# Kernel tuning notes

Hardware: AMD Instinct MI355X
Metric: run time of the kernel (lower is better)

The kernel has to match this reference:

```python
import jax, jax.numpy as jnp
import numpy as np

NUM_Q = 1000
B, T = 64, 100
DK, DV, N = 128, 128, 128

def setup_inputs() -> dict:
    key = jax.random.key(0)
    ks = jax.random.split(key, 12)
    return {
        "q": jax.random.randint(ks[0], (B, T), 0, NUM_Q),
        "r": jax.random.randint(ks[1], (B, T), 0, 2),
        "k_emb": jax.random.normal(ks[2], (NUM_Q, DK), jnp.float32) * 0.1,
        "v_emb": jax.random.normal(ks[3], (2 * NUM_Q, DV), jnp.float32) * 0.1,
        "Mk": jax.random.normal(ks[4], (DK, N), jnp.float32) * 0.1,
        "Mv0": jax.random.normal(ks[5], (N, DV), jnp.float32) * 0.1,
        "f_W": jax.random.normal(ks[6], (2 * DK, DK), jnp.float32) * 0.05,
        "f_b": jnp.zeros((DK,), jnp.float32),
        "p_W": jax.random.normal(ks[7], (DK, 1), jnp.float32) * 0.05,
        "p_b": jnp.zeros((1,), jnp.float32),
        "e_W": jax.random.normal(ks[8], (DV, DV), jnp.float32) * 0.05,
        "e_b": jnp.zeros((DV,), jnp.float32),
        "a_W": jax.random.normal(ks[9], (DV, DV), jnp.float32) * 0.05,
        "a_b": jnp.zeros((DV,), jnp.float32),
    }

def reference(q, r, k_emb, v_emb, Mk, Mv0, f_W, f_b, p_W, p_b, e_W, e_b, a_W, a_b):
    num_q = k_emb.shape[0]
    qr = q + num_q * r                                    # [B,T]
    K = k_emb[q].transpose(1, 0, 2)                       # [T,B,DK]
    V = v_emb[qr].transpose(1, 0, 2)                      # [T,B,DV]
    Mvt0 = jnp.broadcast_to(Mv0, (q.shape[0],) + Mv0.shape)  # [B,N,DV]

    def step(Mvt, kv):
        kt, vt = kv                                       # [B,DK],[B,DV]
        wt = jax.nn.softmax(kt @ Mk, axis=-1)             # [B,N] attention weights
        rt = jnp.einsum('bn,bnd->bd', wt, Mvt)            # memory read
        ft = jnp.tanh(jnp.concatenate([rt, kt], axis=-1) @ f_W + f_b)
        pt = jax.nn.sigmoid(ft @ p_W + p_b)               # [B,1]
        et = jax.nn.sigmoid(vt @ e_W + e_b)               # erase gate [B,DV]
        at = jnp.tanh(vt @ a_W + a_b)                     # add vector [B,DV]
        w_ = wt[:, :, None]                               # [B,N,1]
        Mvt = Mvt * (1.0 - w_ * et[:, None, :]) + w_ * at[:, None, :]
        return Mvt, (pt, Mvt)

    _, (p, Mv) = jax.lax.scan(step, Mvt0, (K, V))         # p: [T,B,1], Mv: [T,B,N,DV]
    p = p.reshape(-1, 1)                                  # cat over time, dim=0 -> [T*B,1]
    Mv = Mv.reshape(-1, Mv.shape[-2], Mv.shape[-1])       # [T*B,N,DV]
    return p, Mv
```

## Files before the change

kernel.cpp:

```cpp
#include <hip/hip_runtime.h>
#include <stdint.h>
#include <stddef.h>


constexpr int B = 64;
constexpr int T = 100;
constexpr int D = 128;
constexpr int NUM_Q = 1000;
constexpr int G = 4;
constexpr int BT = B * T;
constexpr int WSTRIDE = BT * D;

__device__ __forceinline__ float sigmoidf_(float x) {
  return 1.0f / (1.0f + __expf(-x));
}

__global__ __launch_bounds__(128) void kernelA(
    const int* __restrict__ q, const int* __restrict__ r,
    const float* __restrict__ k_emb, const float* __restrict__ v_emb,
    const float* __restrict__ Mk,
    const float* __restrict__ f_W, const float* __restrict__ f_b,
    const float* __restrict__ e_W, const float* __restrict__ e_b,
    const float* __restrict__ a_W, const float* __restrict__ a_b,
    float* __restrict__ ws_w, float* __restrict__ ws_e,
    float* __restrict__ ws_a, float* __restrict__ ws_f)
{
  const int tid = threadIdx.x;
  const int b  = blockIdx.x / (T / G);
  const int tg = blockIdx.x % (T / G);
  const int tbase = tg * G;

  __shared__ float kt[G][D];
  __shared__ float vt[G][D];
  __shared__ float red[D];

  #pragma unroll
  for (int g = 0; g < G; ++g) {
    int idx = b * T + tbase + g;
    int qi  = q[idx];
    int qri = qi + NUM_Q * r[idx];
    kt[g][tid] = k_emb[qi * D + tid];
    vt[g][tid] = v_emb[qri * D + tid];
  }
  __syncthreads();

  float lg[G], se[G], sa[G], sf[G];
  #pragma unroll
  for (int g = 0; g < G; ++g) { lg[g] = 0.f; se[g] = 0.f; sa[g] = 0.f; sf[g] = 0.f; }

  #pragma unroll 4
  for (int k = 0; k < D; ++k) {
    float mk = Mk[k * D + tid];
    float ew = e_W[k * D + tid];
    float aw = a_W[k * D + tid];
    float fw = f_W[(D + k) * D + tid];
    #pragma unroll
    for (int g = 0; g < G; ++g) {
      float kk = kt[g][k];
      float vv = vt[g][k];
      lg[g] = fmaf(kk, mk, lg[g]);
      se[g] = fmaf(vv, ew, se[g]);
      sa[g] = fmaf(vv, aw, sa[g]);
      sf[g] = fmaf(kk, fw, sf[g]);
    }
  }

  const float eb = e_b[tid];
  const float ab = a_b[tid];
  const float fb = f_b[tid];

  for (int g = 0; g < G; ++g) {
    red[tid] = lg[g];
    __syncthreads();
    #pragma unroll
    for (int s = 64; s > 0; s >>= 1) {
      if (tid < s) red[tid] = fmaxf(red[tid], red[tid + s]);
      __syncthreads();
    }
    float mx = red[0];
    __syncthreads();
    float ex = __expf(lg[g] - mx);
    red[tid] = ex;
    __syncthreads();
    #pragma unroll
    for (int s = 64; s > 0; s >>= 1) {
      if (tid < s) red[tid] += red[tid + s];
      __syncthreads();
    }
    float sm = red[0];
    __syncthreads();

    int idx = (b * T + tbase + g) * D + tid;
    ws_w[idx] = ex / sm;
    ws_e[idx] = sigmoidf_(se[g] + eb);
    ws_a[idx] = tanhf(sa[g] + ab);
    ws_f[idx] = sf[g] + fb;
  }
}

__global__ __launch_bounds__(256) void kernelB(
    const float* __restrict__ Mv0,
    const float* __restrict__ ws_w, const float* __restrict__ ws_e,
    const float* __restrict__ ws_a,
    float* __restrict__ out_Mv)
{
  const int b  = blockIdx.x >> 3;
  const int nt = blockIdx.x & 7;
  const int tid = threadIdx.x;
  const int nrow = tid >> 4;
  const int dgrp = tid & 15;
  const int n  = nt * 16 + nrow;
  const int d0 = dgrp * 8;

  float m[8];
  #pragma unroll
  for (int i = 0; i < 8; ++i) m[i] = Mv0[n * D + d0 + i];

  for (int t = 0; t < T; ++t) {
    const int base = (b * T + t) * D;
    float wv = ws_w[base + n];
    const float4* ep = (const float4*)(ws_e + base + d0);
    const float4* ap = (const float4*)(ws_a + base + d0);
    float4 e0 = ep[0], e1 = ep[1];
    float4 a0 = ap[0], a1 = ap[1];
    float ee[8] = {e0.x, e0.y, e0.z, e0.w, e1.x, e1.y, e1.z, e1.w};
    float aa[8] = {a0.x, a0.y, a0.z, a0.w, a1.x, a1.y, a1.z, a1.w};
    #pragma unroll
    for (int i = 0; i < 8; ++i) {
      m[i] = m[i] * (1.0f - wv * ee[i]) + wv * aa[i];
    }
    size_t obase = ((size_t)(t * B + b) * D + n) * D + d0;
    float4 o0 = make_float4(m[0], m[1], m[2], m[3]);
    float4 o1 = make_float4(m[4], m[5], m[6], m[7]);
    *(float4*)(out_Mv + obase)     = o0;
    *(float4*)(out_Mv + obase + 4) = o1;
  }
}

__global__ __launch_bounds__(128) void kernelC(
    const float* __restrict__ Mv0,
    const float* __restrict__ f_W,
    const float* __restrict__ p_W,
    const float* __restrict__ p_b,
    const float* __restrict__ ws_w, const float* __restrict__ ws_f,
    const float* __restrict__ out_Mv,
    float* __restrict__ out_p)
{
  const int bt = blockIdx.x;
  const int b = bt / T;
  const int t = bt % T;
  const int tid = threadIdx.x;

  __shared__ float wsh[D];
  __shared__ float rsh[D];
  __shared__ float red[D];

  const int base = (b * T + t) * D;
  wsh[tid] = ws_w[base + tid];
  __syncthreads();

  const float* Mp = (t == 0)
      ? Mv0
      : (out_Mv + (size_t)((t - 1) * B + b) * (D * D));

  float rt = 0.f;
  #pragma unroll 8
  for (int n = 0; n < D; ++n) rt = fmaf(wsh[n], Mp[n * D + tid], rt);
  rsh[tid] = rt;
  __syncthreads();

  float fa = ws_f[base + tid];
  #pragma unroll 8
  for (int d2 = 0; d2 < D; ++d2) fa = fmaf(rsh[d2], f_W[d2 * D + tid], fa);
  float ft = tanhf(fa);

  red[tid] = ft * p_W[tid];
  __syncthreads();
  #pragma unroll
  for (int s = 64; s > 0; s >>= 1) {
    if (tid < s) red[tid] += red[tid + s];
    __syncthreads();
  }
  if (tid == 0) {
    float pt = sigmoidf_(red[0] + p_b[0]);
    out_p[t * B + b] = pt;
  }
}

extern "C" void kernel_launch(void* const* d_in, const int* in_sizes, int n_in,
                              void* d_out, int out_size, void* d_ws, size_t ws_size,
                              hipStream_t stream)
{
  const int* q = (const int*)d_in[0];
  const int* r = (const int*)d_in[1];
  const float* k_emb = (const float*)d_in[2];
  const float* v_emb = (const float*)d_in[3];
  const float* Mk   = (const float*)d_in[4];
  const float* Mv0  = (const float*)d_in[5];
  const float* f_W  = (const float*)d_in[6];
  const float* f_b  = (const float*)d_in[7];
  const float* p_W  = (const float*)d_in[8];
  const float* p_b  = (const float*)d_in[9];
  const float* e_W  = (const float*)d_in[10];
  const float* e_b  = (const float*)d_in[11];
  const float* a_W  = (const float*)d_in[12];
  const float* a_b  = (const float*)d_in[13];

  float* ws   = (float*)d_ws;
  float* ws_w = ws;
  float* ws_e = ws + (size_t)WSTRIDE;
  float* ws_a = ws + (size_t)2 * WSTRIDE;
  float* ws_f = ws + (size_t)3 * WSTRIDE;

  float* out    = (float*)d_out;
  float* out_p  = out;
  float* out_Mv = out + BT;

  hipLaunchKernelGGL(kernelA, dim3(B * (T / G)), dim3(D), 0, stream,
                     q, r, k_emb, v_emb, Mk, f_W, f_b, e_W, e_b, a_W, a_b,
                     ws_w, ws_e, ws_a, ws_f);
  hipLaunchKernelGGL(kernelB, dim3(B * 8), dim3(256), 0, stream,
                     Mv0, ws_w, ws_e, ws_a, out_Mv);
  hipLaunchKernelGGL(kernelC, dim3(BT), dim3(D), 0, stream,
                     Mv0, f_W, p_W, p_b, ws_w, ws_f, out_Mv, out_p);
}
```

Measured before the change: 604.9 us.

## Fuse memory-read reduction into recurrence kernel and batch the prediction kernel

The recurrence kernel now computes the weighted memory read rt (sum over n of w·Mv) while Mv is still in registers, reducing across lanes with shuffles and shared memory and writing per-tile partial sums to workspace. The prediction kernel then sums those partials instead of re-reading the full previous Mv from global memory, and handles four timesteps per block so f_W loads are shared. Other changes: the next step's w/e/a are prefetched, output stores use nontemporal hints, and the softmax and p reductions use wave shuffles. The cost is a per-step __syncthreads in the recurrence kernel and an extra workspace buffer.

```diff
diff --git a/kernel.cpp b/kernel.cpp
--- a/kernel.cpp
+++ b/kernel.cpp
@@ -8,8 +8,11 @@
 constexpr int D = 128;
 constexpr int NUM_Q = 1000;
 constexpr int G = 4;
+constexpr int CG = 4;
 constexpr int BT = B * T;
 constexpr int WSTRIDE = BT * D;
+
+typedef float v4f __attribute__((ext_vector_type(4)));
 
 __device__ __forceinline__ float sigmoidf_(float x) {
   return 1.0f / (1.0f + __expf(-x));
@@ -32,7 +35,7 @@
 
   __shared__ float kt[G][D];
   __shared__ float vt[G][D];
-  __shared__ float red[D];
+  __shared__ float redm[2], reds[2];
 
   #pragma unroll
   for (int g = 0; g < G; ++g) {
@@ -70,25 +73,19 @@
   const float fb = f_b[tid];
 
   for (int g = 0; g < G; ++g) {
-    red[tid] = lg[g];
+    float v = lg[g];
+    #pragma unroll
+    for (int s = 32; s > 0; s >>= 1) v = fmaxf(v, __shfl_xor(v, s));
+    if ((tid & 63) == 0) redm[tid >> 6] = v;
     __syncthreads();
-    #pragma unroll
-    for (int s = 64; s > 0; s >>= 1) {
-      if (tid < s) red[tid] = fmaxf(red[tid], red[tid + s]);
-      __syncthreads();
-    }
-    float mx = red[0];
+    float mx = fmaxf(redm[0], redm[1]);
+    float ex = __expf(lg[g] - mx);
+    v = ex;
+    #pragma unroll
+    for (int s = 32; s > 0; s >>= 1) v += __shfl_xor(v, s);
+    if ((tid & 63) == 0) reds[tid >> 6] = v;
     __syncthreads();
-    float ex = __expf(lg[g] - mx);
-    red[tid] = ex;
-    __syncthreads();
-    #pragma unroll
-    for (int s = 64; s > 0; s >>= 1) {
-      if (tid < s) red[tid] += red[tid + s];
-      __syncthreads();
-    }
-    float sm = red[0];
-    __syncthreads();
+    float sm = reds[0] + reds[1];
 
     int idx = (b * T + tbase + g) * D + tid;
     ws_w[idx] = ex / sm;
@@ -102,7 +99,7 @@
     const float* __restrict__ Mv0,
     const float* __restrict__ ws_w, const float* __restrict__ ws_e,
     const float* __restrict__ ws_a,
-    float* __restrict__ out_Mv)
+    float* __restrict__ out_Mv, float* __restrict__ ws_rt)
 {
   const int b  = blockIdx.x >> 3;
   const int nt = blockIdx.x & 7;
@@ -111,79 +108,114 @@
   const int dgrp = tid & 15;
   const int n  = nt * 16 + nrow;
   const int d0 = dgrp * 8;
+  const int wave = tid >> 6;
+  const int lane = tid & 63;
+
+  __shared__ float part[2][4][16][8];
 
   float m[8];
   #pragma unroll
   for (int i = 0; i < 8; ++i) m[i] = Mv0[n * D + d0 + i];
 
+  const float*  pw = ws_w + (size_t)(b * T) * D + n;
+  const float4* pe = (const float4*)(ws_e + (size_t)(b * T) * D + d0);
+  const float4* pa = (const float4*)(ws_a + (size_t)(b * T) * D + d0);
+
+  float  wv = pw[0];
+  float4 e0 = pe[0], e1 = pe[1], a0 = pa[0], a1 = pa[1];
+
   for (int t = 0; t < T; ++t) {
-    const int base = (b * T + t) * D;
-    float wv = ws_w[base + n];
-    const float4* ep = (const float4*)(ws_e + base + d0);
-    const float4* ap = (const float4*)(ws_a + base + d0);
-    float4 e0 = ep[0], e1 = ep[1];
-    float4 a0 = ap[0], a1 = ap[1];
+    const int tn = (t + 1 < T) ? (t + 1) : t;
+    float  wn  = pw[(size_t)tn * D];
+    float4 en0 = pe[(size_t)tn * 32], en1 = pe[(size_t)tn * 32 + 1];
+    float4 an0 = pa[(size_t)tn * 32], an1 = pa[(size_t)tn * 32 + 1];
+
+    float pr[8];
+    #pragma unroll
+    for (int i = 0; i < 8; ++i) pr[i] = wv * m[i];
+    #pragma unroll
+    for (int i = 0; i < 8; ++i) {
+      pr[i] += __shfl_xor(pr[i], 16);
+      pr[i] += __shfl_xor(pr[i], 32);
+    }
+    if (lane < 16) {
+      #pragma unroll
+      for (int i = 0; i < 8; ++i) part[t & 1][wave][lane][i] = pr[i];
+    }
+
     float ee[8] = {e0.x, e0.y, e0.z, e0.w, e1.x, e1.y, e1.z, e1.w};
     float aa[8] = {a0.x, a0.y, a0.z, a0.w, a1.x, a1.y, a1.z, a1.w};
     #pragma unroll
     for (int i = 0; i < 8; ++i) {
       m[i] = m[i] * (1.0f - wv * ee[i]) + wv * aa[i];
     }
+
     size_t obase = ((size_t)(t * B + b) * D + n) * D + d0;
-    float4 o0 = make_float4(m[0], m[1], m[2], m[3]);
-    float4 o1 = make_float4(m[4], m[5], m[6], m[7]);
-    *(float4*)(out_Mv + obase)     = o0;
-    *(float4*)(out_Mv + obase + 4) = o1;
+    v4f o0 = {m[0], m[1], m[2], m[3]};
+    v4f o1 = {m[4], m[5], m[6], m[7]};
+    __builtin_nontemporal_store(o0, (v4f*)(out_Mv + obase));
+    __builtin_nontemporal_store(o1, (v4f*)(out_Mv + obase + 4));
+
+    __syncthreads();
+    if (tid < D) {
+      const int dg = tid >> 3, di = tid & 7;
+      float s = part[t & 1][0][dg][di] + part[t & 1][1][dg][di]
+              + part[t & 1][2][dg][di] + part[t & 1][3][dg][di];
+      ws_rt[((size_t)(b * T + t) * 8 + nt) * D + tid] = s;
+    }
+
+    wv = wn; e0 = en0; e1 = en1; a0 = an0; a1 = an1;
   }
 }
 
 __global__ __launch_bounds__(128) void kernelC(
-    const float* __restrict__ Mv0,
     const float* __restrict__ f_W,
     const float* __restrict__ p_W,
     const float* __restrict__ p_b,
-    const float* __restrict__ ws_w, const float* __restrict__ ws_f,
-    const float* __restrict__ out_Mv,
+    const float* __restrict__ ws_f, const float* __restrict__ ws_rt,
     float* __restrict__ out_p)
 {
-  const int bt = blockIdx.x;
-  const int b = bt / T;
-  const int t = bt % T;
+  const int grp = blockIdx.x;
+  const int b  = grp / (T / CG);
+  const int tg = grp % (T / CG);
+  const int t0 = tg * CG;
+  const int bt0 = b * T + t0;
   const int tid = threadIdx.x;
 
-  __shared__ float wsh[D];
-  __shared__ float rsh[D];
-  __shared__ float red[D];
-
-  const int base = (b * T + t) * D;
-  wsh[tid] = ws_w[base + tid];
+  __shared__ float rsh[CG][D];
+  __shared__ float wred[CG][2];
+
+  float fa[CG];
+  #pragma unroll
+  for (int g = 0; g < CG; ++g) {
+    const float* prt = ws_rt + (size_t)(bt0 + g) * (8 * D);
+    float rt = 0.f;
+    #pragma unroll
+    for (int nt = 0; nt < 8; ++nt) rt += prt[nt * D + tid];
+    rsh[g][tid] = rt;
+    fa[g] = ws_f[(bt0 + g) * D + tid];
+  }
   __syncthreads();
 
-  const float* Mp = (t == 0)
-      ? Mv0
-      : (out_Mv + (size_t)((t - 1) * B + b) * (D * D));
-
-  float rt = 0.f;
-  #pragma unroll 8
-  for (int n = 0; n < D; ++n) rt = fmaf(wsh[n], Mp[n * D + tid], rt);
-  rsh[tid] = rt;
+  #pragma unroll 4
+  for (int d2 = 0; d2 < D; ++d2) {
+    float fw = f_W[d2 * D + tid];
+    #pragma unroll
+    for (int g = 0; g < CG; ++g) fa[g] = fmaf(rsh[g][d2], fw, fa[g]);
+  }
+
+  const float pw = p_W[tid];
+  #pragma unroll
+  for (int g = 0; g < CG; ++g) {
+    float v = tanhf(fa[g]) * pw;
+    #pragma unroll
+    for (int s = 32; s > 0; s >>= 1) v += __shfl_xor(v, s);
+    if ((tid & 63) == 0) wred[g][tid >> 6] = v;
+  }
   __syncthreads();
-
-  float fa = ws_f[base + tid];
-  #pragma unroll 8
-  for (int d2 = 0; d2 < D; ++d2) fa = fmaf(rsh[d2], f_W[d2 * D + tid], fa);
-  float ft = tanhf(fa);
-
-  red[tid] = ft * p_W[tid];
-  __syncthreads();
-  #pragma unroll
-  for (int s = 64; s > 0; s >>= 1) {
-    if (tid < s) red[tid] += red[tid + s];
-    __syncthreads();
-  }
-  if (tid == 0) {
-    float pt = sigmoidf_(red[0] + p_b[0]);
-    out_p[t * B + b] = pt;
+  if (tid < CG) {
+    float pt = sigmoidf_(wred[tid][0] + wred[tid][1] + p_b[0]);
+    out_p[(t0 + tid) * B + b] = pt;
   }
 }
 
@@ -211,6 +243,7 @@
   float* ws_e = ws + (size_t)WSTRIDE;
   float* ws_a = ws + (size_t)2 * WSTRIDE;
   float* ws_f = ws + (size_t)3 * WSTRIDE;
+  float* ws_rt = ws + (size_t)4 * WSTRIDE;
 
   float* out    = (float*)d_out;
   float* out_p  = out;
@@ -220,7 +253,7 @@
                      q, r, k_emb, v_emb, Mk, f_W, f_b, e_W, e_b, a_W, a_b,
                      ws_w, ws_e, ws_a, ws_f);
   hipLaunchKernelGGL(kernelB, dim3(B * 8), dim3(256), 0, stream,
-                     Mv0, ws_w, ws_e, ws_a, out_Mv);
-  hipLaunchKernelGGL(kernelC, dim3(BT), dim3(D), 0, stream,
-                     Mv0, f_W, p_W, p_b, ws_w, ws_f, out_Mv, out_p);
-}
+                     Mv0, ws_w, ws_e, ws_a, out_Mv, ws_rt);
+  hipLaunchKernelGGL(kernelC, dim3(B * (T / CG)), dim3(D), 0, stream,
+                     f_W, p_W, p_b, ws_f, ws_rt, out_p);
+}
```

Result: faster. 589.3 us (-2.6%).
